# Kernel tuning notes

Measured on AMD Instinct MI355X. Metric: run time of the kernel, lower is better.

The kernel has to match this reference:

```python
import jax, jax.numpy as jnp
import numpy as np
from jax import lax

B, C, H, W = 8, 128, 64, 64


def conv1x1(x, w):
    # x: [B, Cin, H, W], w: [Cout, Cin] (1x1 conv, no bias)
    return jnp.einsum('oc,bchw->bohw', w, x)


def maxpool2x2(x):
    # 2x2 max pool, stride 2, NCHW
    return lax.reduce_window(x, -jnp.inf, lax.max, (1, 1, 2, 2), (1, 1, 2, 2), 'VALID')


def setup_inputs() -> dict:
    key = jax.random.key(0)
    ks = jax.random.split(key, 5)
    c8, c2 = C // 8, C // 2
    inputs = jax.random.normal(ks[0], (B, C, H, W), dtype=jnp.float32)
    w_theta = jax.random.normal(ks[1], (c8, C), dtype=jnp.float32) * (1.0 / np.sqrt(C))
    w_phi = jax.random.normal(ks[2], (c8, C), dtype=jnp.float32) * (1.0 / np.sqrt(C))
    w_g = jax.random.normal(ks[3], (c2, C), dtype=jnp.float32) * (1.0 / np.sqrt(C))
    w_o = jax.random.normal(ks[4], (C, c2), dtype=jnp.float32) * (1.0 / np.sqrt(c2))
    gamma = jnp.float32(0.1)  # nonzero so attention branch contributes
    return {"inputs": inputs, "w_theta": w_theta, "w_phi": w_phi,
            "w_g": w_g, "w_o": w_o, "gamma": gamma}


def reference(inputs, w_theta, w_phi, w_g, w_o, gamma):
    batch, c, h, w = inputs.shape
    c8, c2 = c // 8, c // 2
    theta = conv1x1(inputs, w_theta).reshape(batch, c8, h * w)            # [B, C/8, HW]
    phi = maxpool2x2(conv1x1(inputs, w_phi)).reshape(batch, c8, -1)       # [B, C/8, HW/4]
    g = maxpool2x2(conv1x1(inputs, w_g)).reshape(batch, c2, -1)           # [B, C/2, HW/4]
    # beta[b, i, j] = softmax_j( theta[b,:,i] . phi[b,:,j] )
    scores = jnp.einsum('bci,bcj->bij', theta, phi)                       # [B, HW, HW/4]
    beta = jax.nn.softmax(scores, axis=-1)
    o = jnp.einsum('bcj,bij->bci', g, beta).reshape(batch, c2, h, w)      # [B, C/2, H, W]
    o = conv1x1(o, w_o)                                                   # [B, C, H, W]
    return gamma * o + inputs
```

## Files before the change

### kernel.cpp

```cpp
#include <hip/hip_runtime.h>
#include <math.h>

#define HW 4096
#define SHIFT 12.0f

typedef __attribute__((ext_vector_type(4)))  short short4v;
typedef __attribute__((ext_vector_type(8)))  short short8;
typedef __attribute__((ext_vector_type(4)))  float f32x4;
typedef __attribute__((ext_vector_type(16))) float f32x16;
typedef __attribute__((ext_vector_type(4)))  int   int4v;

#define MFMA16 __builtin_amdgcn_mfma_f32_16x16x32_bf16
#define MFMA32 __builtin_amdgcn_mfma_f32_32x32x16_bf16

__device__ inline short f2b(float f) {
    union { float f; unsigned u; } v; v.f = f;
    unsigned r = v.u + 0x7fffu + ((v.u >> 16) & 1u);
    return (short)(r >> 16);
}
__device__ inline int pk2(float a, float b) {
    return (int)((unsigned)(unsigned short)f2b(a) |
                 ((unsigned)(unsigned short)f2b(b) << 16));
}

__global__ __launch_bounds__(256) void prep_w(
    const float* __restrict__ wt, const float* __restrict__ wp,
    const float* __restrict__ wg, const float* __restrict__ wo,
    short* __restrict__ wcat, short* __restrict__ wo_blk)
{
    int t = blockIdx.x * 256 + threadIdx.x;
    if (t < 12288) {
        int co = t >> 7, c = t & 127;
        float v = (co < 16) ? wt[co * 128 + c]
                : (co < 32) ? wp[(co - 16) * 128 + c]
                            : wg[(co - 32) * 128 + c];
        wcat[t] = f2b(v);
    } else if (t < 20480) {
        int u = t - 12288;
        int co = u >> 6, c = u & 63;
        wo_blk[((c >> 4) * 128 + co) * 16 + (c & 15)] = f2b(wo[u]);
    }
}

__global__ __launch_bounds__(256) void conv_pool(
    const float* __restrict__ x, const short* __restrict__ wcat,
    short* __restrict__ theta_t, short* __restrict__ phi_t,
    short* __restrict__ g_blk)
{
    __shared__ short xl[128 * 132];
    const int tid = threadIdx.x;
    const int w = tid >> 6, lane = tid & 63, l15 = lane & 15, lg = lane >> 4;
    const int b = blockIdx.x >> 5, rp = blockIdx.x & 31;
    const float* xb = x + (size_t)b * 128 * HW + rp * 128;

    for (int it = 0; it < 16; it++) {
        int idx = it * 256 + tid;
        int c = idx >> 5, p4 = (idx & 31) * 4;
        f32x4 v = *(const f32x4*)(xb + (size_t)c * HW + p4);
        short4v sv = { f2b(v.x), f2b(v.y), f2b(v.z), f2b(v.w) };
        *(short4v*)(xl + c * 132 + p4) = sv;
    }
    __syncthreads();

    f32x4 acc[2][6];
#pragma unroll
    for (int cc = 0; cc < 2; cc++)
#pragma unroll
        for (int cs = 0; cs < 6; cs++) acc[cc][cs] = (f32x4){0.f,0.f,0.f,0.f};

#pragma unroll
    for (int ks = 0; ks < 4; ks++) {
        short8 a[2];
#pragma unroll
        for (int cc = 0; cc < 2; cc++) {
            int px = (w + cc * 4) * 16 + l15;
#pragma unroll
            for (int q = 0; q < 8; q++)
                a[cc][q] = xl[(ks * 32 + lg * 8 + q) * 132 + px];
        }
#pragma unroll
        for (int cs = 0; cs < 6; cs++) {
            short8 bf = *(const short8*)(wcat + (cs * 16 + l15) * 128 + ks * 32 + lg * 8);
            acc[0][cs] = MFMA16(a[0], bf, acc[0][cs], 0, 0, 0);
            acc[1][cs] = MFMA16(a[1], bf, acc[1][cs], 0, 0, 0);
        }
    }

#pragma unroll
    for (int cc = 0; cc < 2; cc++)
#pragma unroll
        for (int r = 0; r < 4; r++) {
            int px = (w + cc * 4) * 16 + lg * 4 + r;
            theta_t[((size_t)b * 4096 + rp * 128 + px) * 16 + l15] = f2b(acc[cc][0][r]);
        }

#pragma unroll
    for (int h = 0; h < 2; h++) {
        float m = fmaxf(fmaxf(acc[0][1][2*h], acc[0][1][2*h+1]),
                        fmaxf(acc[1][1][2*h], acc[1][1][2*h+1]));
        phi_t[((size_t)b * 1024 + rp * 32 + w * 8 + lg * 2 + h) * 16 + l15] = f2b(m);
    }
    const int jb = rp * 2 + (w >> 1), jl = (w & 1) * 8 + lg * 2;
#pragma unroll
    for (int cs = 2; cs < 6; cs++) {
        float m0 = fmaxf(fmaxf(acc[0][cs][0], acc[0][cs][1]),
                         fmaxf(acc[1][cs][0], acc[1][cs][1]));
        float m1 = fmaxf(fmaxf(acc[0][cs][2], acc[0][cs][3]),
                         fmaxf(acc[1][cs][2], acc[1][cs][3]));
        *(int*)(g_blk + (((size_t)b * 64 + jb) * 64 + (cs - 2) * 16 + l15) * 16 + jl)
            = pk2(m0, m1);
    }
}

__global__ __launch_bounds__(256) void attn_k(
    const float* __restrict__ x, const short* __restrict__ theta_t,
    const short* __restrict__ phi_t, const short* __restrict__ g_blk,
    const short* __restrict__ wo_blk, const float* __restrict__ gamma_p,
    float* __restrict__ out)
{
    __shared__ float lds[8192 + 256];
    const int tid = threadIdx.x;
    const int w = tid >> 6, lane = tid & 63, l31 = lane & 31, lam = lane >> 5;
    const int b = blockIdx.x >> 6, i0 = (blockIdx.x & 63) << 6;
    const int ihalf = w & 1, jhalf = w >> 1;
    const int i = i0 + ihalf * 32 + l31;

    short8 tb = *(const short8*)(theta_t + ((size_t)b * 4096 + i) * 16 + lam * 8);

    f32x16 acc0, acc1;
#pragma unroll
    for (int r = 0; r < 16; r++) { acc0[r] = 0.f; acc1[r] = 0.f; }
    float rs = 0.f;
    f32x16 z16;
#pragma unroll
    for (int r = 0; r < 16; r++) z16[r] = 0.f;

    for (int t = 0; t < 8; t++) {
        const int jt = jhalf * 8 + t;
        f32x16 s0, s1;
        {
            short8 pa0 = *(const short8*)(phi_t + ((size_t)b * 1024 + jt * 64 + l31) * 16 + lam * 8);
            short8 pa1 = *(const short8*)(phi_t + ((size_t)b * 1024 + jt * 64 + 32 + l31) * 16 + lam * 8);
            s0 = MFMA32(pa0, tb, z16, 0, 0, 0);
            s1 = MFMA32(pa1, tb, z16, 0, 0, 0);
        }
        int W[16], X[16];
#pragma unroll
        for (int jk = 0; jk < 2; jk++)
#pragma unroll
            for (int rg = 0; rg < 4; rg++)
#pragma unroll
                for (int h = 0; h < 2; h++) {
                    float p0 = __expf((jk ? s1 : s0)[rg * 4 + 2 * h]     - SHIFT);
                    float p1 = __expf((jk ? s1 : s0)[rg * 4 + 2 * h + 1] - SHIFT);
                    rs += p0 + p1;
                    W[jk * 8 + rg * 2 + h] = pk2(p0, p1);
                }
#pragma unroll
        for (int k = 0; k < 16; k++) X[k] = __shfl_xor(W[k], 32, 64);

#pragma unroll
        for (int ck = 0; ck < 4; ck++) {
            const int cb2 = (ck >> 1) * 8 + (ck & 1) * 4;
            int4v pi;
            pi.x = lam ? X[cb2 + 2] : W[cb2];
            pi.y = lam ? X[cb2 + 3] : W[cb2 + 1];
            pi.z = lam ? W[cb2 + 2] : X[cb2];
            pi.w = lam ? W[cb2 + 3] : X[cb2 + 1];
            short8 pb = __builtin_bit_cast(short8, pi);
            const short* gp = g_blk + (((size_t)b * 64 + jt * 4 + ck) * 64) * 16;
            short8 ga0 = *(const short8*)(gp + (l31)      * 16 + lam * 8);
            short8 ga1 = *(const short8*)(gp + (32 + l31) * 16 + lam * 8);
            acc0 = MFMA32(ga0, pb, acc0, 0, 0, 0);
            acc1 = MFMA32(ga1, pb, acc1, 0, 0, 0);
        }
    }

    rs += __shfl_xor(rs, 32, 64);

#pragma unroll
    for (int reg = 0; reg < 16; reg++) {
        lds[((w * 2 + 0) * 16 + reg) * 64 + lane] = acc0[reg];
        lds[((w * 2 + 1) * 16 + reg) * 64 + lane] = acc1[reg];
    }
    lds[8192 + w * 64 + lane] = rs;
    __syncthreads();

    const int cbhalf = w >> 1;
    float o[32];
#pragma unroll
    for (int cs2 = 0; cs2 < 2; cs2++)
#pragma unroll
        for (int reg = 0; reg < 16; reg++)
            o[cs2 * 16 + reg] =
                lds[((ihalf       * 2 + cs2) * 16 + reg) * 64 + lane] +
                lds[(((2 + ihalf) * 2 + cs2) * 16 + reg) * 64 + lane];
    float lf = lds[8192 + ihalf * 64 + lane] + lds[8192 + (2 + ihalf) * 64 + lane];
    float rinv = 1.0f / lf;
#pragma unroll
    for (int k = 0; k < 32; k++) o[k] *= rinv;

    int Wo[16], Xo[16];
#pragma unroll
    for (int cs2 = 0; cs2 < 2; cs2++)
#pragma unroll
        for (int rg = 0; rg < 4; rg++)
#pragma unroll
            for (int h = 0; h < 2; h++)
                Wo[cs2 * 8 + rg * 2 + h] =
                    pk2(o[cs2 * 16 + rg * 4 + 2 * h], o[cs2 * 16 + rg * 4 + 2 * h + 1]);
#pragma unroll
    for (int k = 0; k < 16; k++) Xo[k] = __shfl_xor(Wo[k], 32, 64);

    const float gam = gamma_p[0];
#pragma unroll
    for (int cb = 0; cb < 2; cb++) {
        f32x16 oc;
#pragma unroll
        for (int r = 0; r < 16; r++) oc[r] = 0.f;
#pragma unroll
        for (int kc = 0; kc < 4; kc++) {
            const int cb2 = (kc >> 1) * 8 + (kc & 1) * 4;
            int4v pi;
            pi.x = lam ? Xo[cb2 + 2] : Wo[cb2];
            pi.y = lam ? Xo[cb2 + 3] : Wo[cb2 + 1];
            pi.z = lam ? Wo[cb2 + 2] : Xo[cb2];
            pi.w = lam ? Wo[cb2 + 3] : Xo[cb2 + 1];
            short8 ob = __builtin_bit_cast(short8, pi);
            short8 wa = *(const short8*)(wo_blk +
                ((size_t)(kc * 128 + cbhalf * 64 + cb * 32 + l31)) * 16 + lam * 8);
            oc = MFMA32(wa, ob, oc, 0, 0, 0);
        }
#pragma unroll
        for (int reg = 0; reg < 16; reg++) {
            int co = cbhalf * 64 + cb * 32 + (reg & 3) + 8 * (reg >> 2) + 4 * lam;
            size_t idx = ((size_t)b * 128 + co) * HW + i0 + ihalf * 32 + l31;
            out[idx] = gam * oc[reg] + x[idx];
        }
    }
}

extern "C" void kernel_launch(void* const* d_in, const int* in_sizes, int n_in,
                              void* d_out, int out_size, void* d_ws, size_t ws_size,
                              hipStream_t stream)
{
    const float* x     = (const float*)d_in[0];
    const float* wt    = (const float*)d_in[1];
    const float* wp    = (const float*)d_in[2];
    const float* wg    = (const float*)d_in[3];
    const float* wo    = (const float*)d_in[4];
    const float* gamma = (const float*)d_in[5];
    float* out = (float*)d_out;

    char* ws = (char*)d_ws;
    short* wcat    = (short*)(ws + 0);
    short* wo_blk  = (short*)(ws + 24576);
    short* theta_t = (short*)(ws + 40960);
    short* phi_t   = (short*)(ws + 1089536);
    short* g_blk   = (short*)(ws + 1351680);

    prep_w   <<<80,  256, 0, stream>>>(wt, wp, wg, wo, wcat, wo_blk);
    conv_pool<<<256, 256, 0, stream>>>(x, wcat, theta_t, phi_t, g_blk);
    attn_k   <<<512, 256, 0, stream>>>(x, theta_t, phi_t, g_blk, wo_blk, gamma, out);
}
```

Baseline: 113.8 us.

## Fuse conv/pool and attention into one cooperative kernel with grid sync

Merges the weight-prep, conv+pool and attention kernels into a single cooperative launch of 512 blocks that runs the projection phase, syncs the whole grid, then runs attention. Phase 1 is reworked to 512 blocks of half-width pixel tiles, each wave computing three output-channel groups. It converts fp32 weights to bf16 inline instead of running a separate prep kernel. The goal is to remove two kernel launches and the gaps between them. In exchange it adds grid-sync cost, redundant per-block weight conversion, and a two-kernel fallback if the cooperative launch fails.

```diff
diff --git a/kernel.cpp b/kernel.cpp
--- a/kernel.cpp
+++ b/kernel.cpp
@@ -1,5 +1,8 @@
 #include <hip/hip_runtime.h>
+#include <hip/hip_cooperative_groups.h>
 #include <math.h>
+
+namespace cg = cooperative_groups;
 
 #define HW 4096
 #define SHIFT 12.0f
@@ -22,118 +25,116 @@
     return (int)((unsigned)(unsigned short)f2b(a) |
                  ((unsigned)(unsigned short)f2b(b) << 16));
 }
-
-__global__ __launch_bounds__(256) void prep_w(
-    const float* __restrict__ wt, const float* __restrict__ wp,
-    const float* __restrict__ wg, const float* __restrict__ wo,
-    short* __restrict__ wcat, short* __restrict__ wo_blk)
-{
-    int t = blockIdx.x * 256 + threadIdx.x;
-    if (t < 12288) {
-        int co = t >> 7, c = t & 127;
-        float v = (co < 16) ? wt[co * 128 + c]
-                : (co < 32) ? wp[(co - 16) * 128 + c]
-                            : wg[(co - 32) * 128 + c];
-        wcat[t] = f2b(v);
-    } else if (t < 20480) {
-        int u = t - 12288;
-        int co = u >> 6, c = u & 63;
-        wo_blk[((c >> 4) * 128 + co) * 16 + (c & 15)] = f2b(wo[u]);
-    }
-}
-
-__global__ __launch_bounds__(256) void conv_pool(
-    const float* __restrict__ x, const short* __restrict__ wcat,
-    short* __restrict__ theta_t, short* __restrict__ phi_t,
-    short* __restrict__ g_blk)
-{
-    __shared__ short xl[128 * 132];
+__device__ inline short8 ld8(const float* p) {
+    f32x4 a = *(const f32x4*)p;
+    f32x4 b = *(const f32x4*)(p + 4);
+    short8 r;
+    r[0] = f2b(a.x); r[1] = f2b(a.y); r[2] = f2b(a.z); r[3] = f2b(a.w);
+    r[4] = f2b(b.x); r[5] = f2b(b.y); r[6] = f2b(b.z); r[7] = f2b(b.w);
+    return r;
+}
+__device__ inline float max4(float a, float b, float c, float d) {
+    return fmaxf(fmaxf(a, b), fmaxf(c, d));
+}
+
+__device__ void phase1(const float* __restrict__ x, const float* __restrict__ wt,
+                       const float* __restrict__ wp, const float* __restrict__ wg,
+                       short* __restrict__ theta_t, short* __restrict__ phi_t,
+                       short* __restrict__ g_blk, char* smem, int bid)
+{
+    short* xl = (short*)smem;
     const int tid = threadIdx.x;
-    const int w = tid >> 6, lane = tid & 63, l15 = lane & 15, lg = lane >> 4;
-    const int b = blockIdx.x >> 5, rp = blockIdx.x & 31;
-    const float* xb = x + (size_t)b * 128 * HW + rp * 128;
-
-    for (int it = 0; it < 16; it++) {
+    const int w = tid >> 6, lane = tid & 63, l15 = lane & 15, lg = (lane >> 4) & 3;
+    const int b = bid >> 6, ri = bid & 63, rp = ri >> 1, h = ri & 1;
+    const float* xb = x + (size_t)b * 128 * HW + rp * 128 + h * 32;
+
+    for (int it = 0; it < 8; it++) {
         int idx = it * 256 + tid;
-        int c = idx >> 5, p4 = (idx & 31) * 4;
-        f32x4 v = *(const f32x4*)(xb + (size_t)c * HW + p4);
+        int c = idx >> 4, q = idx & 15;
+        int px4 = q * 4, r = px4 >> 5, col4 = px4 & 31;
+        f32x4 v = *(const f32x4*)(xb + (size_t)c * HW + r * 64 + col4);
         short4v sv = { f2b(v.x), f2b(v.y), f2b(v.z), f2b(v.w) };
-        *(short4v*)(xl + c * 132 + p4) = sv;
+        *(short4v*)(xl + c * 68 + px4) = sv;
     }
     __syncthreads();
 
-    f32x4 acc[2][6];
+    const int p = w & 1, csbase = (w >> 1) * 3;
+    f32x4 acc[2][3];
 #pragma unroll
     for (int cc = 0; cc < 2; cc++)
 #pragma unroll
-        for (int cs = 0; cs < 6; cs++) acc[cc][cs] = (f32x4){0.f,0.f,0.f,0.f};
+        for (int cl = 0; cl < 3; cl++) acc[cc][cl] = (f32x4){0.f, 0.f, 0.f, 0.f};
 
 #pragma unroll
     for (int ks = 0; ks < 4; ks++) {
         short8 a[2];
 #pragma unroll
         for (int cc = 0; cc < 2; cc++) {
-            int px = (w + cc * 4) * 16 + l15;
+            int px = (p + 2 * cc) * 16 + l15;
 #pragma unroll
             for (int q = 0; q < 8; q++)
-                a[cc][q] = xl[(ks * 32 + lg * 8 + q) * 132 + px];
-        }
-#pragma unroll
-        for (int cs = 0; cs < 6; cs++) {
-            short8 bf = *(const short8*)(wcat + (cs * 16 + l15) * 128 + ks * 32 + lg * 8);
-            acc[0][cs] = MFMA16(a[0], bf, acc[0][cs], 0, 0, 0);
-            acc[1][cs] = MFMA16(a[1], bf, acc[1][cs], 0, 0, 0);
-        }
-    }
-
-#pragma unroll
-    for (int cc = 0; cc < 2; cc++)
-#pragma unroll
-        for (int r = 0; r < 4; r++) {
-            int px = (w + cc * 4) * 16 + lg * 4 + r;
-            theta_t[((size_t)b * 4096 + rp * 128 + px) * 16 + l15] = f2b(acc[cc][0][r]);
-        }
-
-#pragma unroll
-    for (int h = 0; h < 2; h++) {
-        float m = fmaxf(fmaxf(acc[0][1][2*h], acc[0][1][2*h+1]),
-                        fmaxf(acc[1][1][2*h], acc[1][1][2*h+1]));
-        phi_t[((size_t)b * 1024 + rp * 32 + w * 8 + lg * 2 + h) * 16 + l15] = f2b(m);
-    }
-    const int jb = rp * 2 + (w >> 1), jl = (w & 1) * 8 + lg * 2;
-#pragma unroll
-    for (int cs = 2; cs < 6; cs++) {
-        float m0 = fmaxf(fmaxf(acc[0][cs][0], acc[0][cs][1]),
-                         fmaxf(acc[1][cs][0], acc[1][cs][1]));
-        float m1 = fmaxf(fmaxf(acc[0][cs][2], acc[0][cs][3]),
-                         fmaxf(acc[1][cs][2], acc[1][cs][3]));
-        *(int*)(g_blk + (((size_t)b * 64 + jb) * 64 + (cs - 2) * 16 + l15) * 16 + jl)
-            = pk2(m0, m1);
-    }
-}
-
-__global__ __launch_bounds__(256) void attn_k(
-    const float* __restrict__ x, const short* __restrict__ theta_t,
-    const short* __restrict__ phi_t, const short* __restrict__ g_blk,
-    const short* __restrict__ wo_blk, const float* __restrict__ gamma_p,
-    float* __restrict__ out)
-{
-    __shared__ float lds[8192 + 256];
+                a[cc][q] = xl[(ks * 32 + lg * 8 + q) * 68 + px];
+        }
+#pragma unroll
+        for (int csl = 0; csl < 3; csl++) {
+            int cs = csbase + csl;
+            const float* wrow;
+            if (cs == 0)      wrow = wt + l15 * 128;
+            else if (cs == 1) wrow = wp + l15 * 128;
+            else              wrow = wg + ((cs - 2) * 16 + l15) * 128;
+            short8 bf = ld8(wrow + ks * 32 + lg * 8);
+            acc[0][csl] = MFMA16(a[0], bf, acc[0][csl], 0, 0, 0);
+            acc[1][csl] = MFMA16(a[1], bf, acc[1][csl], 0, 0, 0);
+        }
+    }
+
+    const size_t pixb = (size_t)b * 4096 + rp * 128 + h * 32 + p * 16;
+#pragma unroll
+    for (int csl = 0; csl < 3; csl++) {
+        int cs = csbase + csl;
+        if (cs == 0) {
+#pragma unroll
+            for (int cc = 0; cc < 2; cc++)
+#pragma unroll
+                for (int r = 0; r < 4; r++)
+                    theta_t[(pixb + cc * 64 + lg * 4 + r) * 16 + l15] =
+                        f2b(acc[cc][csl][r]);
+        } else if (cs == 1) {
+#pragma unroll
+            for (int h2 = 0; h2 < 2; h2++) {
+                float m = max4(acc[0][csl][2 * h2], acc[0][csl][2 * h2 + 1],
+                               acc[1][csl][2 * h2], acc[1][csl][2 * h2 + 1]);
+                int j = rp * 32 + h * 16 + p * 8 + lg * 2 + h2;
+                phi_t[((size_t)b * 1024 + j) * 16 + l15] = f2b(m);
+            }
+        } else {
+            int gcrow = (cs - 2) * 16 + l15;
+            float m0 = max4(acc[0][csl][0], acc[0][csl][1], acc[1][csl][0], acc[1][csl][1]);
+            float m1 = max4(acc[0][csl][2], acc[0][csl][3], acc[1][csl][2], acc[1][csl][3]);
+            int jb = rp * 2 + h, jl = p * 8 + lg * 2;
+            *(int*)(g_blk + (((size_t)b * 64 + jb) * 64 + gcrow) * 16 + jl) = pk2(m0, m1);
+        }
+    }
+}
+
+__device__ void phase2(const float* __restrict__ x, const short* __restrict__ theta_t,
+                       const short* __restrict__ phi_t, const short* __restrict__ g_blk,
+                       const float* __restrict__ wo, const float* __restrict__ gamma_p,
+                       float* __restrict__ out, char* smem, int bid)
+{
+    float* lds = (float*)smem;
     const int tid = threadIdx.x;
     const int w = tid >> 6, lane = tid & 63, l31 = lane & 31, lam = lane >> 5;
-    const int b = blockIdx.x >> 6, i0 = (blockIdx.x & 63) << 6;
+    const int b = bid >> 6, i0 = (bid & 63) << 6;
     const int ihalf = w & 1, jhalf = w >> 1;
     const int i = i0 + ihalf * 32 + l31;
 
     short8 tb = *(const short8*)(theta_t + ((size_t)b * 4096 + i) * 16 + lam * 8);
 
-    f32x16 acc0, acc1;
-#pragma unroll
-    for (int r = 0; r < 16; r++) { acc0[r] = 0.f; acc1[r] = 0.f; }
+    f32x16 acc0, acc1, z16;
+#pragma unroll
+    for (int r = 0; r < 16; r++) { acc0[r] = 0.f; acc1[r] = 0.f; z16[r] = 0.f; }
     float rs = 0.f;
-    f32x16 z16;
-#pragma unroll
-    for (int r = 0; r < 16; r++) z16[r] = 0.f;
 
     for (int t = 0; t < 8; t++) {
         const int jt = jhalf * 8 + t;
@@ -227,8 +228,7 @@
             pi.z = lam ? Wo[cb2 + 2] : Xo[cb2];
             pi.w = lam ? Wo[cb2 + 3] : Xo[cb2 + 1];
             short8 ob = __builtin_bit_cast(short8, pi);
-            short8 wa = *(const short8*)(wo_blk +
-                ((size_t)(kc * 128 + cbhalf * 64 + cb * 32 + l31)) * 16 + lam * 8);
+            short8 wa = ld8(wo + (size_t)(cbhalf * 64 + cb * 32 + l31) * 64 + kc * 16 + lam * 8);
             oc = MFMA32(wa, ob, oc, 0, 0, 0);
         }
 #pragma unroll
@@ -238,6 +238,33 @@
             out[idx] = gam * oc[reg] + x[idx];
         }
     }
+}
+
+__global__ __launch_bounds__(256) void fused_k(
+    const float* x, const float* wt, const float* wp, const float* wg,
+    const float* wo, const float* gamma_p, float* out,
+    short* theta_t, short* phi_t, short* g_blk)
+{
+    __shared__ __align__(16) char smem[33792];
+    phase1(x, wt, wp, wg, theta_t, phi_t, g_blk, smem, blockIdx.x);
+    cg::this_grid().sync();
+    phase2(x, theta_t, phi_t, g_blk, wo, gamma_p, out, smem, blockIdx.x);
+}
+
+__global__ __launch_bounds__(256) void p1_k(
+    const float* x, const float* wt, const float* wp, const float* wg,
+    short* theta_t, short* phi_t, short* g_blk)
+{
+    __shared__ __align__(16) char smem[17408];
+    phase1(x, wt, wp, wg, theta_t, phi_t, g_blk, smem, blockIdx.x);
+}
+
+__global__ __launch_bounds__(256) void p2_k(
+    const float* x, const short* theta_t, const short* phi_t, const short* g_blk,
+    const float* wo, const float* gamma_p, float* out)
+{
+    __shared__ __align__(16) char smem[33792];
+    phase2(x, theta_t, phi_t, g_blk, wo, gamma_p, out, smem, blockIdx.x);
 }
 
 extern "C" void kernel_launch(void* const* d_in, const int* in_sizes, int n_in,
@@ -253,13 +280,18 @@
     float* out = (float*)d_out;
 
     char* ws = (char*)d_ws;
-    short* wcat    = (short*)(ws + 0);
-    short* wo_blk  = (short*)(ws + 24576);
-    short* theta_t = (short*)(ws + 40960);
-    short* phi_t   = (short*)(ws + 1089536);
-    short* g_blk   = (short*)(ws + 1351680);
-
-    prep_w   <<<80,  256, 0, stream>>>(wt, wp, wg, wo, wcat, wo_blk);
-    conv_pool<<<256, 256, 0, stream>>>(x, wcat, theta_t, phi_t, g_blk);
-    attn_k   <<<512, 256, 0, stream>>>(x, theta_t, phi_t, g_blk, wo_blk, gamma, out);
-}
+    short* theta_t = (short*)(ws + 0);
+    short* phi_t   = (short*)(ws + 1048576);
+    short* g_blk   = (short*)(ws + 1310720);
+
+    void* args[] = { (void*)&x, (void*)&wt, (void*)&wp, (void*)&wg, (void*)&wo,
+                     (void*)&gamma, (void*)&out, (void*)&theta_t, (void*)&phi_t,
+                     (void*)&g_blk };
+    hipError_t rc = hipLaunchCooperativeKernel((const void*)fused_k,
+                                               dim3(512), dim3(256), args, 0, stream);
+    if (rc != hipSuccess) {
+        (void)hipGetLastError();
+        p1_k<<<512, 256, 0, stream>>>(x, wt, wp, wg, theta_t, phi_t, g_blk);
+        p2_k<<<512, 256, 0, stream>>>(x, theta_t, phi_t, g_blk, wo, gamma, out);
+    }
+}
```

New measurement: 194.2 us. 70.7% more time.
